# Kernel tuning notes

Measured on AMD Instinct MI355X. Metric: run time of the kernel, lower is better.

The kernel has to match this reference:

```python
import jax, jax.numpy as jnp
import numpy as np

DIM = 1024
N_HEADS = 16
HEAD_DIM = DIM // N_HEADS
ROPE_BASE = 10000.0


def setup_inputs() -> dict:
    key = jax.random.key(0)
    ks = jax.random.split(key, 5)
    B, T = 4, 2048
    s_in = 1.0 / np.sqrt(DIM)
    x = jax.random.normal(ks[0], (B, T, DIM), dtype=jnp.float32)
    W_qkv = jax.random.uniform(ks[1], (DIM, 3 * DIM), jnp.float32, -s_in, s_in)
    b_qkv = jax.random.uniform(ks[2], (3 * DIM,), jnp.float32, -s_in, s_in)
    W_proj = jax.random.uniform(ks[3], (DIM, DIM), jnp.float32, -s_in, s_in)
    b_proj = jax.random.uniform(ks[4], (DIM,), jnp.float32, -s_in, s_in)
    return {"x": x, "W_qkv": W_qkv, "b_qkv": b_qkv, "W_proj": W_proj, "b_proj": b_proj}


def _rope_cos_sin(T, dtype):
    inv_freq = 1.0 / (ROPE_BASE ** (jnp.arange(0, HEAD_DIM, 2, dtype=jnp.float32) / HEAD_DIM))
    t = jnp.arange(T, dtype=jnp.float32)
    freqs = jnp.outer(t, inv_freq)            # (T, HEAD_DIM/2)
    emb = jnp.concatenate([freqs, freqs], -1)  # (T, HEAD_DIM)
    return jnp.cos(emb).astype(dtype), jnp.sin(emb).astype(dtype)


def _rotate_half(x):
    x1, x2 = jnp.split(x, 2, axis=-1)
    return jnp.concatenate([-x2, x1], axis=-1)


def reference(x, W_qkv, b_qkv, W_proj, b_proj):
    B, T, C = x.shape
    qkv = x @ W_qkv + b_qkv                              # (B, T, 3C)
    qkv = qkv.reshape(B, T, 3, N_HEADS, HEAD_DIM)
    qkv = jnp.transpose(qkv, (2, 0, 3, 1, 4))            # (3, B, H, T, d)
    q, k, v = qkv[0], qkv[1], qkv[2]
    cos, sin = _rope_cos_sin(T, x.dtype)
    cos = cos[None, None]                                # (1,1,T,d)
    sin = sin[None, None]
    q = q * cos + _rotate_half(q) * sin
    k = k * cos + _rotate_half(k) * sin
    scale = 1.0 / np.sqrt(HEAD_DIM)
    scores = jnp.einsum('bhqd,bhkd->bhqk', q, k) * scale  # (B,H,T,T)
    attn = jax.nn.softmax(scores, axis=-1)
    out = jnp.einsum('bhqk,bhkd->bhqd', attn, v)          # (B,H,T,d)
    out = jnp.transpose(out, (0, 2, 1, 3)).reshape(B, T, C)
    return out @ W_proj + b_proj
```

## Files before the change

kernel.cpp:

```cpp
#include <hip/hip_runtime.h>
#include <hip/hip_bf16.h>
#include <cstdint>
#include <cstddef>

typedef __bf16 bf16x8 __attribute__((ext_vector_type(8)));
typedef float f32x4 __attribute__((ext_vector_type(4)));
typedef float f32x16 __attribute__((ext_vector_type(16)));
typedef unsigned short ushort8 __attribute__((ext_vector_type(8)));

#define MFMA16(a, b, c) __builtin_amdgcn_mfma_f32_16x16x32_bf16(a, b, c, 0, 0, 0)
#define MFMA32(a, b, c) __builtin_amdgcn_mfma_f32_32x32x16_bf16(a, b, c, 0, 0, 0)

__device__ __forceinline__ void gll16(const void* g, void* l) {
  __builtin_amdgcn_global_load_lds((__attribute__((address_space(1))) unsigned int*)g,
                                   (__attribute__((address_space(3))) unsigned int*)l,
                                   16, 0, 0);
}

__device__ __forceinline__ float exp2_raw(float x) {
  return __builtin_amdgcn_exp2f(x);
}

__device__ __forceinline__ bf16x8 pack8(float a0, float a1, float a2, float a3,
                                        float a4, float a5, float a6, float a7) {
  unsigned w0, w1, w2, w3;
  asm("v_cvt_pk_bf16_f32 %0, %1, %2" : "=v"(w0) : "v"(a0), "v"(a1));
  asm("v_cvt_pk_bf16_f32 %0, %1, %2" : "=v"(w1) : "v"(a2), "v"(a3));
  asm("v_cvt_pk_bf16_f32 %0, %1, %2" : "=v"(w2) : "v"(a4), "v"(a5));
  asm("v_cvt_pk_bf16_f32 %0, %1, %2" : "=v"(w3) : "v"(a6), "v"(a7));
  asm("v_permlane32_swap_b32 %0, %1" : "+v"(w0), "+v"(w2));
  asm("v_permlane32_swap_b32 %0, %1" : "+v"(w1), "+v"(w3));
  union { unsigned u[4]; bf16x8 v; } r;
  r.u[0] = w0; r.u[1] = w1; r.u[2] = w2; r.u[3] = w3;
  return r.v;
}


__global__ void cvt_x(const float* __restrict__ in, __bf16* __restrict__ out,
                      float2* __restrict__ tab) {
  int i = (blockIdx.x * 256 + threadIdx.x) * 8;
  float4 a = *(const float4*)(in + i);
  float4 c = *(const float4*)(in + i + 4);
  bf16x8 r;
  r[0] = (__bf16)a.x; r[1] = (__bf16)a.y; r[2] = (__bf16)a.z; r[3] = (__bf16)a.w;
  r[4] = (__bf16)c.x; r[5] = (__bf16)c.y; r[6] = (__bf16)c.z; r[7] = (__bf16)c.w;
  *(bf16x8*)(out + i) = r;
  if (blockIdx.x < 256) {
    int idx = blockIdx.x * 256 + threadIdx.x;
    int t = idx >> 5, ii = idx & 31;
    float invf = exp2f(-(float)ii * (13.287712379549449f / 32.0f));
    float ang = (float)t * invf;
    tab[idx] = make_float2(cosf(ang), sinf(ang));
  }
}

__global__ void transp_w(const float* __restrict__ Wq, __bf16* __restrict__ Wtq,
                         const float* __restrict__ Wp, __bf16* __restrict__ Wtp) {
  __shared__ float tile[32][33];
  int bx = blockIdx.x;
  const float* W; __bf16* Wt; int N;
  if (bx < 96) { W = Wq; Wt = Wtq; N = 3072; }
  else         { W = Wp; Wt = Wtp; N = 1024; bx -= 96; }
  const int K = 1024;
  int n0 = bx * 32, k0 = blockIdx.y * 32;
  int tx = threadIdx.x & 31, ty = threadIdx.x >> 5;
  #pragma unroll
  for (int r = ty; r < 32; r += 8)
    tile[r][tx] = W[(size_t)(k0 + r) * N + n0 + tx];
  __syncthreads();
  #pragma unroll
  for (int r = ty; r < 32; r += 8)
    Wt[(size_t)(n0 + r) * K + k0 + tx] = (__bf16)tile[tx][r];
}

template <int EPI>
__global__ __launch_bounds__(256, 3) void gemm_bt(
    const __bf16* __restrict__ A, const __bf16* __restrict__ Bt,
    const float* __restrict__ bias, float* __restrict__ Cf,
    __bf16* __restrict__ qp, __bf16* __restrict__ kp, __bf16* __restrict__ vtp,
    const float2* __restrict__ ctab, int M, int N, int K) {
  __shared__ __align__(16) char smem[49152];
  const int tid = threadIdx.x;
  const int w = tid >> 6, l = tid & 63, l15 = l & 15, g = l >> 4;
  const int wr = w >> 1, wc = w & 1;
  const int brow = blockIdx.y * 128, bcol = blockIdx.x * 128;

  f32x4 acc[4][4] = {};
  const int rsub = tid >> 3;
  const int sf   = (rsub & 7) ^ (((rsub >> 3) & 3) << 1);
  const int schunk = (((tid & 7) ^ sf) << 4);
  const int fr0 = (l15 & 7) ^ (((l15 >> 3) & 3) << 1);
  const int fr1 = (l15 & 7) ^ ((((l15 >> 3) + 2) & 3) << 1);

  for (int kt = 0; kt < K; kt += 64) {
    __syncthreads();
    #pragma unroll
    for (int i = 0; i < 4; ++i) {
      const char* ga = (const char*)(A + (size_t)(brow + i * 32 + rsub) * K + kt) + schunk;
      gll16(ga, smem + i * 4096 + tid * 16);
      const char* gb = (const char*)(Bt + (size_t)(bcol + i * 32 + rsub) * K + kt) + schunk;
      gll16(gb, smem + 16384 + i * 4096 + tid * 16);
    }
    __syncthreads();
    #pragma unroll
    for (int kk = 0; kk < 2; ++kk) {
      bf16x8 af[4], bfr[4];
      #pragma unroll
      for (int m = 0; m < 4; ++m) {
        int fx = (m & 1) ? fr1 : fr0;
        af[m] = *(const bf16x8*)(smem + (wr * 64 + m * 16 + l15) * 128 +
                                 (((kk * 4 + g) ^ fx) << 4));
      }
      #pragma unroll
      for (int n = 0; n < 4; ++n) {
        int fx = (n & 1) ? fr1 : fr0;
        bfr[n] = *(const bf16x8*)(smem + 16384 + (wc * 64 + n * 16 + l15) * 128 +
                                  (((kk * 4 + g) ^ fx) << 4));
      }
      __builtin_amdgcn_s_setprio(1);
      #pragma unroll
      for (int m = 0; m < 4; ++m)
        #pragma unroll
        for (int n = 0; n < 4; ++n)
          acc[m][n] = MFMA16(af[m], bfr[n], acc[m][n]);
      __builtin_amdgcn_s_setprio(0);
    }
  }

  const int colb = bcol + wc * 64;
  float bs[4];
  #pragma unroll
  for (int n = 0; n < 4; ++n) bs[n] = bias[colb + n * 16 + l15];

  if (EPI == 1) {
    #pragma unroll
    for (int m = 0; m < 4; ++m)
      #pragma unroll
      for (int j = 0; j < 4; ++j) {
        int row = brow + wr * 64 + m * 16 + g * 4 + j;
        float* crow = Cf + (size_t)row * N + colb;
        #pragma unroll
        for (int n = 0; n < 4; ++n)
          crow[n * 16 + l15] = acc[m][n][j] + bs[n];
      }
  } else {
    const int which = colb >> 10;
    if (which < 2) {
      const int h = (colb & 1023) >> 6;
      __bf16* dst = (which == 0) ? qp : kp;
      const float SCLQ = 0.18033688011112042f;
      #pragma unroll
      for (int m = 0; m < 4; ++m)
        #pragma unroll
        for (int j = 0; j < 4; ++j) {
          int row = brow + wr * 64 + m * 16 + g * 4 + j;
          int bb = row >> 11, t = row & 2047;
          float v0 = acc[m][0][j] + bs[0];
          float v1 = acc[m][1][j] + bs[1];
          float v2 = acc[m][2][j] + bs[2];
          float v3 = acc[m][3][j] + bs[3];
          float2 cs0 = ctab[t * 32 + l15];
          float2 cs1 = ctab[t * 32 + 16 + l15];
          float r0 = v0 * cs0.x - v2 * cs0.y;
          float r2 = v2 * cs0.x + v0 * cs0.y;
          float r1 = v1 * cs1.x - v3 * cs1.y;
          float r3 = v3 * cs1.x + v1 * cs1.y;
          v0 = r0; v1 = r1; v2 = r2; v3 = r3;
          if (which == 0) { v0 *= SCLQ; v1 *= SCLQ; v2 *= SCLQ; v3 *= SCLQ; }
          __bf16* orow = dst + ((size_t)(bb * 16 + h) * 2048 + t) * 64;
          orow[l15]      = (__bf16)v0;
          orow[16 + l15] = (__bf16)v1;
          orow[32 + l15] = (__bf16)v2;
          orow[48 + l15] = (__bf16)v3;
        }
    } else {
      __syncthreads();
      #pragma unroll
      for (int n = 0; n < 4; ++n) {
        int cloc = wc * 64 + n * 16 + l15;
        char* cbase = smem + cloc * 256;
        int sw = (cloc & 15) << 4;
        #pragma unroll
        for (int m = 0; m < 4; ++m)
          #pragma unroll
          for (int j = 0; j < 4; ++j) {
            int rloc = wr * 64 + m * 16 + g * 4 + j;
            *(__bf16*)(cbase + ((rloc * 2) ^ sw)) = (__bf16)(acc[m][n][j] + bs[n]);
          }
      }
      __syncthreads();
      const int b = brow >> 11, t0 = brow & 2047;
      const int h0 = (bcol - 2048) >> 6;
      const int tch = l & 15;
      #pragma unroll
      for (int i = 0; i < 8; ++i) {
        int c = w * 32 + i * 4 + (l >> 4);
        ushort8 vrow = *(const ushort8*)(smem + c * 256 + ((tch * 16) ^ ((c & 15) << 4)));
        __bf16* dst = vtp + ((size_t)((b * 16 + h0 + (c >> 6)) * 64 + (c & 63)) * 2048 +
                             t0 + tch * 8);
        *(ushort8*)dst = vrow;
      }
    }
  }
}

__global__ __launch_bounds__(256, 4) void flash_attn(
    const __bf16* __restrict__ q, const __bf16* __restrict__ k,
    const __bf16* __restrict__ vt, __bf16* __restrict__ o) {
  __shared__ __align__(16) char smem[32768];
  const int id = blockIdx.x;
  const int nid = (id & 7) * 128 + (id >> 3);
  const int bh = nid >> 4, qb = nid & 15;
  const int b = bh >> 4, h = bh & 15;
  const int tid = threadIdx.x, w = tid >> 6, l = tid & 63;
  const int l31 = l & 31, hi = l >> 5;

  const char* kbase  = (const char*)(k  + (size_t)bh * 2048 * 64);
  const char* vtbase = (const char*)(vt + (size_t)bh * 64 * 2048);

  bf16x8 qf[4];
  const int qrow0 = qb * 128 + w * 32;
  #pragma unroll
  for (int ks = 0; ks < 4; ++ks)
    qf[ks] = *(const bf16x8*)(q + (size_t)bh * 2048 * 64 +
                              (size_t)(qrow0 + l31) * 64 + ks * 16 + hi * 8);

  f32x16 accO[2] = {};
  float lr = 0.f;

  const int koff[2] = { 0, 16384 };
  const int voff[2] = { 8192, 24576 };

  const int srow = tid >> 3;
  const int ssw  = (((tid & 7) ^ ((tid >> 3) & 7) ^ (((tid >> 6) & 3) << 1)) << 4);
  const int swz  = (((l & 7) ^ (((l >> 3) & 3) << 1)) << 4);

  gll16(kbase + srow * 128 + ssw,                  smem + koff[0] + tid * 16);
  gll16(kbase + (srow + 32) * 128 + ssw,           smem + koff[0] + 4096 + tid * 16);
  gll16(vtbase + (size_t)srow * 4096 + ssw,        smem + voff[0] + tid * 16);
  gll16(vtbase + (size_t)(srow + 32) * 4096 + ssw, smem + voff[0] + 4096 + tid * 16);
  __syncthreads();

  for (int t = 0; t < 32; ++t) {
    const int cur = t & 1;
    char* Kc = smem + koff[cur];
    char* Vc = smem + voff[cur];
    if (t < 31) {
      char* Kn = smem + koff[cur ^ 1];
      char* Vn = smem + voff[cur ^ 1];
      const char* gk = kbase + (size_t)(t + 1) * 8192;
      gll16(gk + srow * 128 + ssw,        Kn + tid * 16);
      gll16(gk + (srow + 32) * 128 + ssw, Kn + 4096 + tid * 16);
      const char* gv = vtbase + (size_t)(t + 1) * 128;
      gll16(gv + (size_t)srow * 4096 + ssw,        Vn + tid * 16);
      gll16(gv + (size_t)(srow + 32) * 4096 + ssw, Vn + 4096 + tid * 16);
    }

    f32x16 st0 = {}, st1 = {};
    __builtin_amdgcn_s_setprio(1);
    #pragma unroll
    for (int ks = 0; ks < 4; ++ks) {
      bf16x8 kf0 = *(const bf16x8*)(Kc + (l31) * 128 + ((ks * 32 + hi * 16) ^ swz));
      bf16x8 kf1 = *(const bf16x8*)(Kc + (32 + l31) * 128 + ((ks * 32 + hi * 16) ^ swz));
      st0 = MFMA32(kf0, qf[ks], st0);
      st1 = MFMA32(kf1, qf[ks], st1);
    }
    __builtin_amdgcn_s_setprio(0);

    bf16x8 pa[4];
    {
      float p[16];
      #pragma unroll
      for (int r = 0; r < 16; ++r) p[r] = exp2_raw(st0[r]);
      lr += (((p[0] + p[1]) + (p[2] + p[3])) + ((p[4] + p[5]) + (p[6] + p[7]))) +
            (((p[8] + p[9]) + (p[10] + p[11])) + ((p[12] + p[13]) + (p[14] + p[15])));
      pa[0] = pack8(p[0], p[1], p[2], p[3], p[4], p[5], p[6], p[7]);
      pa[1] = pack8(p[8], p[9], p[10], p[11], p[12], p[13], p[14], p[15]);
    }
    {
      float p[16];
      #pragma unroll
      for (int r = 0; r < 16; ++r) p[r] = exp2_raw(st1[r]);
      lr += (((p[0] + p[1]) + (p[2] + p[3])) + ((p[4] + p[5]) + (p[6] + p[7]))) +
            (((p[8] + p[9]) + (p[10] + p[11])) + ((p[12] + p[13]) + (p[14] + p[15])));
      pa[2] = pack8(p[0], p[1], p[2], p[3], p[4], p[5], p[6], p[7]);
      pa[3] = pack8(p[8], p[9], p[10], p[11], p[12], p[13], p[14], p[15]);
    }

    __builtin_amdgcn_s_setprio(1);
    #pragma unroll
    for (int ks = 0; ks < 4; ++ks) {
      bf16x8 vf0 = *(const bf16x8*)(Vc + (l31) * 128 + ((ks * 32 + hi * 16) ^ swz));
      bf16x8 vf1 = *(const bf16x8*)(Vc + (32 + l31) * 128 + ((ks * 32 + hi * 16) ^ swz));
      accO[0] = MFMA32(pa[ks], vf0, accO[0]);
      accO[1] = MFMA32(pa[ks], vf1, accO[1]);
    }
    __builtin_amdgcn_s_setprio(0);
    __syncthreads();
  }

  float lrf = lr + __shfl_xor(lr, 32);
  __bf16* obase = o + (size_t)(b * 2048) * 1024 + h * 64;
  #pragma unroll
  for (int r = 0; r < 16; ++r) {
    int qloc = (r & 3) + 8 * (r >> 2) + 4 * hi;
    float inv = 1.0f / __shfl(lrf, qloc);
    __bf16* orow = obase + (size_t)(qrow0 + qloc) * 1024;
    orow[l31]      = (__bf16)(accO[0][r] * inv);
    orow[32 + l31] = (__bf16)(accO[1][r] * inv);
  }
}


extern "C" void kernel_launch(void* const* d_in, const int* in_sizes, int n_in,
                              void* d_out, int out_size, void* d_ws, size_t ws_size,
                              hipStream_t stream) {
  const float* x     = (const float*)d_in[0];
  const float* Wqkv  = (const float*)d_in[1];
  const float* bqkv  = (const float*)d_in[2];
  const float* Wproj = (const float*)d_in[3];
  const float* bproj = (const float*)d_in[4];
  float* out = (float*)d_out;

  char* ws = (char*)d_ws;
  __bf16* xb  = (__bf16*)(ws);
  __bf16* wtq = (__bf16*)(ws + 16777216);
  __bf16* wtp = (__bf16*)(ws + 23068672);
  __bf16* qp  = (__bf16*)(ws + 25165824);
  __bf16* kp  = (__bf16*)(ws + 41943040);
  __bf16* vtp = (__bf16*)(ws + 58720256);
  __bf16* ao  = (__bf16*)(ws + 75497472);
  float2* ct  = (float2*)(ws + 92274688);
  if (ws_size < 92798976) return;

  cvt_x<<<4096, 256, 0, stream>>>(x, xb, ct);
  transp_w<<<dim3(128, 32), 256, 0, stream>>>(Wqkv, wtq, Wproj, wtp);
  gemm_bt<0><<<dim3(24, 64), 256, 0, stream>>>(xb, wtq, bqkv, nullptr, qp, kp, vtp, ct,
                                               8192, 3072, 1024);
  flash_attn<<<1024, 256, 0, stream>>>(qp, kp, vtp, ao);
  gemm_bt<1><<<dim3(8, 64), 256, 0, stream>>>(ao, wtp, bproj, out, nullptr, nullptr,
                                              nullptr, nullptr, 8192, 1024, 1024);
}
```

Before: 177.2 us.

## Process two query tiles per flash-attention block to reuse K/V tiles

```diff
diff --git a/kernel.cpp b/kernel.cpp
--- a/kernel.cpp
+++ b/kernel.cpp
@@ -204,13 +204,13 @@
   }
 }
 
-__global__ __launch_bounds__(256, 4) void flash_attn(
+__global__ __launch_bounds__(256, 2) void flash_attn(
     const __bf16* __restrict__ q, const __bf16* __restrict__ k,
     const __bf16* __restrict__ vt, __bf16* __restrict__ o) {
   __shared__ __align__(16) char smem[32768];
   const int id = blockIdx.x;
-  const int nid = (id & 7) * 128 + (id >> 3);
-  const int bh = nid >> 4, qb = nid & 15;
+  const int nid = (id & 7) * 64 + (id >> 3);
+  const int bh = nid >> 3, qb = nid & 7;
   const int b = bh >> 4, h = bh & 15;
   const int tid = threadIdx.x, w = tid >> 6, l = tid & 63;
   const int l31 = l & 31, hi = l >> 5;
@@ -218,15 +218,19 @@
   const char* kbase  = (const char*)(k  + (size_t)bh * 2048 * 64);
   const char* vtbase = (const char*)(vt + (size_t)bh * 64 * 2048);
 
-  bf16x8 qf[4];
-  const int qrow0 = qb * 128 + w * 32;
-  #pragma unroll
-  for (int ks = 0; ks < 4; ++ks)
-    qf[ks] = *(const bf16x8*)(q + (size_t)bh * 2048 * 64 +
-                              (size_t)(qrow0 + l31) * 64 + ks * 16 + hi * 8);
-
-  f32x16 accO[2] = {};
-  float lr = 0.f;
+  bf16x8 qfa[4], qfb[4];
+  const int qrow0a = qb * 256 + w * 32;
+  const int qrow0b = qrow0a + 128;
+  #pragma unroll
+  for (int ks = 0; ks < 4; ++ks) {
+    qfa[ks] = *(const bf16x8*)(q + (size_t)bh * 2048 * 64 +
+                               (size_t)(qrow0a + l31) * 64 + ks * 16 + hi * 8);
+    qfb[ks] = *(const bf16x8*)(q + (size_t)bh * 2048 * 64 +
+                               (size_t)(qrow0b + l31) * 64 + ks * 16 + hi * 8);
+  }
+
+  f32x16 accA[2] = {}, accB[2] = {};
+  float lra = 0.f, lrb = 0.f;
 
   const int koff[2] = { 0, 16384 };
   const int voff[2] = { 8192, 24576 };
@@ -256,35 +260,55 @@
       gll16(gv + (size_t)(srow + 32) * 4096 + ssw, Vn + 4096 + tid * 16);
     }
 
-    f32x16 st0 = {}, st1 = {};
+    f32x16 sa0 = {}, sa1 = {}, sb0 = {}, sb1 = {};
     __builtin_amdgcn_s_setprio(1);
     #pragma unroll
     for (int ks = 0; ks < 4; ++ks) {
       bf16x8 kf0 = *(const bf16x8*)(Kc + (l31) * 128 + ((ks * 32 + hi * 16) ^ swz));
       bf16x8 kf1 = *(const bf16x8*)(Kc + (32 + l31) * 128 + ((ks * 32 + hi * 16) ^ swz));
-      st0 = MFMA32(kf0, qf[ks], st0);
-      st1 = MFMA32(kf1, qf[ks], st1);
+      sa0 = MFMA32(kf0, qfa[ks], sa0);
+      sa1 = MFMA32(kf1, qfa[ks], sa1);
+      sb0 = MFMA32(kf0, qfb[ks], sb0);
+      sb1 = MFMA32(kf1, qfb[ks], sb1);
     }
     __builtin_amdgcn_s_setprio(0);
 
-    bf16x8 pa[4];
+    bf16x8 paa[4], pab[4];
     {
       float p[16];
       #pragma unroll
-      for (int r = 0; r < 16; ++r) p[r] = exp2_raw(st0[r]);
-      lr += (((p[0] + p[1]) + (p[2] + p[3])) + ((p[4] + p[5]) + (p[6] + p[7]))) +
-            (((p[8] + p[9]) + (p[10] + p[11])) + ((p[12] + p[13]) + (p[14] + p[15])));
-      pa[0] = pack8(p[0], p[1], p[2], p[3], p[4], p[5], p[6], p[7]);
-      pa[1] = pack8(p[8], p[9], p[10], p[11], p[12], p[13], p[14], p[15]);
+      for (int r = 0; r < 16; ++r) p[r] = exp2_raw(sa0[r]);
+      lra += (((p[0] + p[1]) + (p[2] + p[3])) + ((p[4] + p[5]) + (p[6] + p[7]))) +
+             (((p[8] + p[9]) + (p[10] + p[11])) + ((p[12] + p[13]) + (p[14] + p[15])));
+      paa[0] = pack8(p[0], p[1], p[2], p[3], p[4], p[5], p[6], p[7]);
+      paa[1] = pack8(p[8], p[9], p[10], p[11], p[12], p[13], p[14], p[15]);
     }
     {
       float p[16];
       #pragma unroll
-      for (int r = 0; r < 16; ++r) p[r] = exp2_raw(st1[r]);
-      lr += (((p[0] + p[1]) + (p[2] + p[3])) + ((p[4] + p[5]) + (p[6] + p[7]))) +
-            (((p[8] + p[9]) + (p[10] + p[11])) + ((p[12] + p[13]) + (p[14] + p[15])));
-      pa[2] = pack8(p[0], p[1], p[2], p[3], p[4], p[5], p[6], p[7]);
-      pa[3] = pack8(p[8], p[9], p[10], p[11], p[12], p[13], p[14], p[15]);
+      for (int r = 0; r < 16; ++r) p[r] = exp2_raw(sa1[r]);
+      lra += (((p[0] + p[1]) + (p[2] + p[3])) + ((p[4] + p[5]) + (p[6] + p[7]))) +
+             (((p[8] + p[9]) + (p[10] + p[11])) + ((p[12] + p[13]) + (p[14] + p[15])));
+      paa[2] = pack8(p[0], p[1], p[2], p[3], p[4], p[5], p[6], p[7]);
+      paa[3] = pack8(p[8], p[9], p[10], p[11], p[12], p[13], p[14], p[15]);
+    }
+    {
+      float p[16];
+      #pragma unroll
+      for (int r = 0; r < 16; ++r) p[r] = exp2_raw(sb0[r]);
+      lrb += (((p[0] + p[1]) + (p[2] + p[3])) + ((p[4] + p[5]) + (p[6] + p[7]))) +
+             (((p[8] + p[9]) + (p[10] + p[11])) + ((p[12] + p[13]) + (p[14] + p[15])));
+      pab[0] = pack8(p[0], p[1], p[2], p[3], p[4], p[5], p[6], p[7]);
+      pab[1] = pack8(p[8], p[9], p[10], p[11], p[12], p[13], p[14], p[15]);
+    }
+    {
+      float p[16];
+      #pragma unroll
+      for (int r = 0; r < 16; ++r) p[r] = exp2_raw(sb1[r]);
+      lrb += (((p[0] + p[1]) + (p[2] + p[3])) + ((p[4] + p[5]) + (p[6] + p[7]))) +
+             (((p[8] + p[9]) + (p[10] + p[11])) + ((p[12] + p[13]) + (p[14] + p[15])));
+      pab[2] = pack8(p[0], p[1], p[2], p[3], p[4], p[5], p[6], p[7]);
+      pab[3] = pack8(p[8], p[9], p[10], p[11], p[12], p[13], p[14], p[15]);
     }
 
     __builtin_amdgcn_s_setprio(1);
@@ -292,22 +316,29 @@
     for (int ks = 0; ks < 4; ++ks) {
       bf16x8 vf0 = *(const bf16x8*)(Vc + (l31) * 128 + ((ks * 32 + hi * 16) ^ swz));
       bf16x8 vf1 = *(const bf16x8*)(Vc + (32 + l31) * 128 + ((ks * 32 + hi * 16) ^ swz));
-      accO[0] = MFMA32(pa[ks], vf0, accO[0]);
-      accO[1] = MFMA32(pa[ks], vf1, accO[1]);
+      accA[0] = MFMA32(paa[ks], vf0, accA[0]);
+      accA[1] = MFMA32(paa[ks], vf1, accA[1]);
+      accB[0] = MFMA32(pab[ks], vf0, accB[0]);
+      accB[1] = MFMA32(pab[ks], vf1, accB[1]);
     }
     __builtin_amdgcn_s_setprio(0);
     __syncthreads();
   }
 
-  float lrf = lr + __shfl_xor(lr, 32);
+  float lrfa = lra + __shfl_xor(lra, 32);
+  float lrfb = lrb + __shfl_xor(lrb, 32);
   __bf16* obase = o + (size_t)(b * 2048) * 1024 + h * 64;
   #pragma unroll
   for (int r = 0; r < 16; ++r) {
     int qloc = (r & 3) + 8 * (r >> 2) + 4 * hi;
-    float inv = 1.0f / __shfl(lrf, qloc);
-    __bf16* orow = obase + (size_t)(qrow0 + qloc) * 1024;
-    orow[l31]      = (__bf16)(accO[0][r] * inv);
-    orow[32 + l31] = (__bf16)(accO[1][r] * inv);
+    float inva = 1.0f / __shfl(lrfa, qloc);
+    float invb = 1.0f / __shfl(lrfb, qloc);
+    __bf16* orowa = obase + (size_t)(qrow0a + qloc) * 1024;
+    __bf16* orowb = obase + (size_t)(qrow0b + qloc) * 1024;
+    orowa[l31]      = (__bf16)(accA[0][r] * inva);
+    orowa[32 + l31] = (__bf16)(accA[1][r] * inva);
+    orowb[l31]      = (__bf16)(accB[0][r] * invb);
+    orowb[32 + l31] = (__bf16)(accB[1][r] * invb);
   }
 }
 
@@ -337,7 +368,7 @@
   transp_w<<<dim3(128, 32), 256, 0, stream>>>(Wqkv, wtq, Wproj, wtp);
   gemm_bt<0><<<dim3(24, 64), 256, 0, stream>>>(xb, wtq, bqkv, nullptr, qp, kp, vtp, ct,
                                                8192, 3072, 1024);
-  flash_attn<<<1024, 256, 0, stream>>>(qp, kp, vtp, ao);
+  flash_attn<<<512, 256, 0, stream>>>(qp, kp, vtp, ao);
   gemm_bt<1><<<dim3(8, 64), 256, 0, stream>>>(ao, wtp, bproj, out, nullptr, nullptr,
                                               nullptr, nullptr, 8192, 1024, 1024);
 }
```

Result: faster. 170.3 us (-3.9%).
